# Performance work log

Measured on AMD Instinct MI355X. Metric: run time of the kernel, lower is better.

Reference implementation:

```python
import jax, jax.numpy as jnp
import numpy as np

NUM_GRAPHS = 5 * 0 + 64  # number of graphs in the batch
NUM_CLASSES = 5


def gcn_conv(x, src, dst, W, b, n_nodes):
    """PyG GCNConv: x' = D^{-1/2} (A+I) D^{-1/2} x W + b (self-loops already in src/dst)."""
    h = x @ W  # [N, out]
    deg = jax.ops.segment_sum(jnp.ones(dst.shape, h.dtype), dst, num_segments=n_nodes)
    dinv = deg ** -0.5  # deg >= 1 thanks to self-loops
    norm = dinv[src] * dinv[dst]  # [E+N]
    msg = h[src] * norm[:, None]  # gather + normalize
    out = jax.ops.segment_sum(msg, dst, num_segments=n_nodes)  # scatter-add
    return out + b


def setup_inputs() -> dict:
    key = jax.random.key(0)
    ks = jax.random.split(key, 12)
    N, E, D_IN, D_H, D_F = 50000, 500000, 128, 256, 256
    x = jax.random.normal(ks[0], (N, D_IN), dtype=jnp.float32)
    edge_index = jax.random.randint(ks[1], (2, E), 0, N, dtype=jnp.int64)
    batch = jnp.sort(jax.random.randint(ks[2], (N,), 0, NUM_GRAPHS, dtype=jnp.int64))
    def lin(k, fi, fo):
        s = 1.0 / np.sqrt(fi)
        return jax.random.uniform(k, (fi, fo), jnp.float32, -s, s)
    return {
        "x": x, "edge_index": edge_index, "batch": batch,
        "W0": lin(ks[3], D_IN, D_H), "b0": jnp.zeros((D_H,), jnp.float32),
        "W1": lin(ks[4], D_H, D_H),  "b1": jnp.zeros((D_H,), jnp.float32),
        "W2": lin(ks[5], D_H, D_H),  "b2": jnp.zeros((D_H,), jnp.float32),
        "Wc1": lin(ks[6], D_H, D_F), "bc1": jnp.zeros((D_F,), jnp.float32),
        "Wc2": lin(ks[7], D_F, NUM_CLASSES), "bc2": jnp.zeros((NUM_CLASSES,), jnp.float32),
    }


def reference(x, edge_index, batch, W0, b0, W1, b1, W2, b2, Wc1, bc1, Wc2, bc2):
    n_nodes = x.shape[0]
    loops = jnp.arange(n_nodes, dtype=edge_index.dtype)
    src = jnp.concatenate([edge_index[0], loops])
    dst = jnp.concatenate([edge_index[1], loops])

    h = jax.nn.relu(gcn_conv(x, src, dst, W0, b0, n_nodes))
    h = jax.nn.relu(gcn_conv(h, src, dst, W1, b1, n_nodes))
    h = jax.nn.relu(gcn_conv(h, src, dst, W2, b2, n_nodes))

    # global_mean_pool over batch ids
    sums = jax.ops.segment_sum(h, batch, num_segments=NUM_GRAPHS)
    cnts = jax.ops.segment_sum(jnp.ones((n_nodes,), h.dtype), batch, num_segments=NUM_GRAPHS)
    g = sums / jnp.maximum(cnts, 1.0)[:, None]  # [NUM_GRAPHS, D_H]

    # classifier MLP (dropout inactive at eval)
    out = jax.nn.relu(g @ Wc1 + bc1) @ Wc2 + bc2
    return out
```

## Files before the change

kernel.cpp:

```cpp
#include <hip/hip_runtime.h>
#include <hip/hip_fp16.h>

typedef _Float16 f16x8 __attribute__((ext_vector_type(8)));
typedef float fx4 __attribute__((ext_vector_type(4)));

#define AS_G(p) ((const __attribute__((address_space(1))) void*)(p))
#define AS_L(p) ((__attribute__((address_space(3))) void*)(p))

struct __align__(8) half4 { __half2 lo, hi; };
struct __align__(8) edge_t { int u; float w; };

__device__ inline void split2h(float a, __half& hi, __half& lo) {
    hi = __float2half(a);
    lo = __float2half(a - __half2float(hi));
}


__global__ void k_degx(const int* __restrict__ dst, int E, int* __restrict__ deg, int degB,
                       const float* __restrict__ x, __half* __restrict__ xh, int nx) {
    if (blockIdx.x < (unsigned)degB) {
        int i = (blockIdx.x * 256 + threadIdx.x) * 4;
        if (i + 4 <= E) {
            int4 d4 = *(const int4*)&dst[i];
            atomicAdd(&deg[d4.x], 1);
            atomicAdd(&deg[d4.y], 1);
            atomicAdd(&deg[d4.z], 1);
            atomicAdd(&deg[d4.w], 1);
        } else {
            for (int j = i; j < E; ++j) atomicAdd(&deg[dst[j]], 1);
        }
    } else {
        int i = (blockIdx.x - degB) * 1024 + threadIdx.x * 4;
        if (i < nx) {
            float4 v = *(const float4*)&x[i];
            __half2 h0(__float2half(v.x), __float2half(v.y));
            __half2 h1(__float2half(v.z), __float2half(v.w));
            *(__half2*)&xh[i] = h0;
            *(__half2*)&xh[i + 2] = h1;
        }
    }
}

__global__ void k_scan1w(const int* __restrict__ deg, int N, int nb,
                         int* __restrict__ part, int* __restrict__ bsum, float* __restrict__ dinv,
                         const float* __restrict__ W0, __half* __restrict__ h0, __half* __restrict__ l0,
                         const float* __restrict__ W1, __half* __restrict__ h1, __half* __restrict__ l1,
                         const float* __restrict__ W2, __half* __restrict__ h2, __half* __restrict__ l2,
                         int DIN, int DH) {
    __shared__ int s[256];
    if (blockIdx.x < (unsigned)nb) {
        int i = blockIdx.x * 256 + threadIdx.x;
        int v = (i < N) ? deg[i] : 0;
        if (i < N) dinv[i] = 1.0f / sqrtf((float)(v + 1));
        s[threadIdx.x] = v;
        __syncthreads();
        for (int off = 1; off < 256; off <<= 1) {
            int t = (threadIdx.x >= off) ? s[threadIdx.x - off] : 0;
            __syncthreads();
            s[threadIdx.x] += t;
            __syncthreads();
        }
        if (i < N) part[i] = s[threadIdx.x] - v;
        if (threadIdx.x == 255) bsum[blockIdx.x] = s[255];
    } else {
        int i = (blockIdx.x - nb) * 256 + threadIdx.x;
        const int n0 = DIN * DH, n1 = DH * DH;
        const float* W; __half *hT, *lT; int K, li;
        if (i < n0) { W = W0; hT = h0; lT = l0; K = DIN; li = i; }
        else if (i < n0 + n1) { W = W1; hT = h1; lT = l1; K = DH; li = i - n0; }
        else if (i < n0 + 2 * n1) { W = W2; hT = h2; lT = l2; K = DH; li = i - n0 - n1; }
        else return;
        int k = li / DH, n = li - k * DH;
        __half h, l;
        split2h(W[li], h, l);
        hT[(size_t)n * K + k] = h;
        lT[(size_t)n * K + k] = l;
    }
}

__global__ void k_scan3(const int* __restrict__ part, const int* __restrict__ bsum, int nb,
                        int N, int E, int* __restrict__ rowptr, int* __restrict__ cursor) {
    __shared__ int s[256];
    const int t = threadIdx.x;
    s[t] = (t < nb && t < (int)blockIdx.x) ? bsum[t] : 0;
    __syncthreads();
    for (int off = 128; off > 0; off >>= 1) {
        if (t < off) s[t] += s[t + off];
        __syncthreads();
    }
    const int base = s[0];
    int i = blockIdx.x * 256 + t;
    if (i < N) {
        int v = part[i] + base;
        rowptr[i] = v;
        cursor[i] = v;
    }
    if (i == 0) rowptr[N] = E;
}

__global__ void k_fill(const int* __restrict__ src, const int* __restrict__ dst, int E,
                       const float* __restrict__ dinv, int* __restrict__ cursor,
                       edge_t* __restrict__ edg) {
    int e = blockIdx.x * blockDim.x + threadIdx.x;
    if (e < E) {
        int s = src[e], d = dst[e];
        int p = atomicAdd(&cursor[d], 1);
        edge_t ed;
        ed.u = s;
        ed.w = dinv[s] * dinv[d];
        edg[p] = ed;
    }
}


__device__ __forceinline__ void gemm_core(
    const __half* __restrict__ Aop, const __half* __restrict__ BhiT, const __half* __restrict__ BloT,
    __half* smem, int Nrows, int K, int row0,
    int wid, int lane, int wrow, int wcol, int quad, int l16, fx4 (&acc)[4][4]) {
    const __half* gp[5];
    int ldsoff[5];
#pragma unroll
    for (int j = 0; j < 5; ++j) {
        int L = wid * 5 + j;
        int arr, slot;
        if (L < 8) { arr = 0; slot = L; }
        else if (L < 24) { arr = 1; slot = L - 8; }
        else { arr = 2; slot = L - 24; }
        int r = 16 * slot + (lane >> 2);
        int s = lane & 3;
        int q = (s - (r >> 1)) & 3;
        const __half* garr = (arr == 0) ? Aop : (arr == 1) ? BhiT : BloT;
        int grow = (arr == 0) ? min(row0 + r, Nrows - 1) : r;
        gp[j] = garr + (size_t)grow * K + q * 8;
        ldsoff[j] = ((arr == 0) ? 0 : (arr == 1) ? 8192 : 24576) + slot * 1024;
    }

    const __half* sA   = smem;
    const __half* sBhi = smem + 4096;
    const __half* sBlo = smem + 12288;

    int aidx[4], bidx[4];
#pragma unroll
    for (int t = 0; t < 4; ++t) {
        int ra = wrow * 64 + t * 16 + l16;
        aidx[t] = ra * 32 + ((quad + (ra >> 1)) & 3) * 8;
        int rb = wcol * 64 + t * 16 + l16;
        bidx[t] = rb * 32 + ((quad + (rb >> 1)) & 3) * 8;
    }

    for (int k0 = 0; k0 < K; k0 += 32) {
#pragma unroll
        for (int j = 0; j < 5; ++j)
            __builtin_amdgcn_global_load_lds(AS_G(gp[j] + k0), AS_L((char*)smem + ldsoff[j]), 16, 0, 0);
        __syncthreads();

        f16x8 a[4];
#pragma unroll
        for (int mi = 0; mi < 4; ++mi) a[mi] = *(const f16x8*)&sA[aidx[mi]];
#pragma unroll
        for (int nj = 0; nj < 4; ++nj) {
            f16x8 bh = *(const f16x8*)&sBhi[bidx[nj]];
            f16x8 bl = *(const f16x8*)&sBlo[bidx[nj]];
#pragma unroll
            for (int mi = 0; mi < 4; ++mi) {
                acc[mi][nj] = __builtin_amdgcn_mfma_f32_16x16x32_f16(a[mi], bh, acc[mi][nj], 0, 0, 0);
                acc[mi][nj] = __builtin_amdgcn_mfma_f32_16x16x32_f16(a[mi], bl, acc[mi][nj], 0, 0, 0);
            }
        }
        __syncthreads();
    }
}

__global__ __launch_bounds__(512) void k_gemm_mfma(
    const __half* __restrict__ Aop, const __half* __restrict__ BhiT, const __half* __restrict__ BloT,
    const float* __restrict__ bias, __half* __restrict__ C, int Nrows, int K) {
    __shared__ __align__(16) __half smem[20480];
    const int tid = threadIdx.x;
    const int wid = tid >> 6, lane = tid & 63;
    const int row0 = blockIdx.x * 128;
    const int wrow = wid & 1, wcol = wid >> 1;
    const int quad = lane >> 4, l16 = lane & 15;

    fx4 acc[4][4] = {};
    gemm_core(Aop, BhiT, BloT, smem, Nrows, K, row0, wid, lane, wrow, wcol, quad, l16, acc);

#pragma unroll
    for (int mi = 0; mi < 4; ++mi) {
        const int rbase = row0 + wrow * 64 + mi * 16 + quad * 4;
#pragma unroll
        for (int nj = 0; nj < 4; ++nj) {
            const int c = wcol * 64 + nj * 16 + l16;
            const float bc = bias[c];
#pragma unroll
            for (int reg = 0; reg < 4; ++reg) {
                int r = rbase + reg;
                if (r < Nrows) C[(size_t)r * 256 + c] = __float2half(fmaxf(acc[mi][nj][reg] + bc, 0.f));
            }
        }
    }
}

__global__ __launch_bounds__(512) void k_gemm_pool(
    const __half* __restrict__ Aop, const __half* __restrict__ BhiT, const __half* __restrict__ BloT,
    const float* __restrict__ bias, const int* __restrict__ batch,
    float* __restrict__ gsum, int Nrows, int K) {
    __shared__ __align__(16) __half smem[20480];
    const int tid = threadIdx.x;
    const int wid = tid >> 6, lane = tid & 63;
    const int row0 = blockIdx.x * 128;
    const int wrow = wid & 1, wcol = wid >> 1;
    const int quad = lane >> 4, l16 = lane & 15;

    fx4 acc[4][4] = {};
    gemm_core(Aop, BhiT, BloT, smem, Nrows, K, row0, wid, lane, wrow, wcol, quad, l16, acc);

    int bg[4][4];
#pragma unroll
    for (int mi = 0; mi < 4; ++mi)
#pragma unroll
        for (int reg = 0; reg < 4; ++reg) {
            int r = row0 + wrow * 64 + mi * 16 + quad * 4 + reg;
            bg[mi][reg] = (r < Nrows) ? batch[r] : -1;
        }
    const int gfirst = batch[row0 < Nrows ? row0 : (Nrows - 1)];
    const int glast  = batch[min(row0 + 127, Nrows - 1)];

#pragma unroll
    for (int nj = 0; nj < 4; ++nj) {
        const int c = wcol * 64 + nj * 16 + l16;
        const float bc = bias[c];
        for (int g = gfirst; g <= glast; ++g) {
            float s = 0.f;
#pragma unroll
            for (int mi = 0; mi < 4; ++mi)
#pragma unroll
                for (int reg = 0; reg < 4; ++reg)
                    if (bg[mi][reg] == g) s += fmaxf(acc[mi][nj][reg] + bc, 0.f);
            s += __shfl_xor(s, 16);
            s += __shfl_xor(s, 32);
            if (quad == 0) atomicAdd(&gsum[g * 256 + c], s);
        }
    }
}


__global__ __launch_bounds__(256) void k_agg256(const __half* __restrict__ H, const int* __restrict__ rowptr,
                                                const edge_t* __restrict__ edg,
                                                const float* __restrict__ dinv,
                                                __half* __restrict__ outA, int N) {
    const int wave = threadIdx.x >> 6, lane = threadIdx.x & 63;
    const int nw = gridDim.x * 4;
    for (int v = blockIdx.x * 4 + wave; v < N; v += nw) {
        const float di = dinv[v];
        const float selfn = di * di;
        half4 hv = ((const half4*)&H[(size_t)v * 256])[lane];
        float2 s0 = __half22float2(hv.lo), s1 = __half22float2(hv.hi);
        float ax = selfn * s0.x, ay = selfn * s0.y, az = selfn * s1.x, aw = selfn * s1.y;

        int e = rowptr[v];
        const int end = rowptr[v + 1];
        for (; e + 8 <= end; e += 8) {
            edge_t ed[8]; half4 g[8];
#pragma unroll
            for (int j = 0; j < 8; ++j) ed[j] = edg[e + j];
#pragma unroll
            for (int j = 0; j < 8; ++j) g[j] = ((const half4*)&H[(size_t)ed[j].u * 256])[lane];
#pragma unroll
            for (int j = 0; j < 8; ++j) {
                float2 f0 = __half22float2(g[j].lo), f1 = __half22float2(g[j].hi);
                ax += ed[j].w * f0.x; ay += ed[j].w * f0.y; az += ed[j].w * f1.x; aw += ed[j].w * f1.y;
            }
        }
        for (; e < end; ++e) {
            edge_t ed = edg[e];
            half4 g = ((const half4*)&H[(size_t)ed.u * 256])[lane];
            float2 f0 = __half22float2(g.lo), f1 = __half22float2(g.hi);
            ax += ed.w * f0.x; ay += ed.w * f0.y; az += ed.w * f1.x; aw += ed.w * f1.y;
        }

        half4 o;
        o.lo = __floats2half2_rn(ax, ay);
        o.hi = __floats2half2_rn(az, aw);
        ((half4*)outA)[(size_t)v * 64 + lane] = o;
    }
}

__global__ __launch_bounds__(256) void k_agg128(const __half* __restrict__ X, const int* __restrict__ rowptr,
                                                const edge_t* __restrict__ edg,
                                                const float* __restrict__ dinv,
                                                __half* __restrict__ outA, int N) {
    const int half = threadIdx.x >> 5, sub = threadIdx.x & 31;
    const int nw = gridDim.x * 8;
    for (int v = blockIdx.x * 8 + half; v < N; v += nw) {
        const float di = dinv[v];
        const float selfn = di * di;
        half4 hv = ((const half4*)&X[(size_t)v * 128])[sub];
        float2 s0 = __half22float2(hv.lo), s1 = __half22float2(hv.hi);
        float ax = selfn * s0.x, ay = selfn * s0.y, az = selfn * s1.x, aw = selfn * s1.y;

        int e = rowptr[v];
        const int end = rowptr[v + 1];
        for (; e + 4 <= end; e += 4) {
            edge_t ed[4]; half4 g[4];
#pragma unroll
            for (int j = 0; j < 4; ++j) ed[j] = edg[e + j];
#pragma unroll
            for (int j = 0; j < 4; ++j) g[j] = ((const half4*)&X[(size_t)ed[j].u * 128])[sub];
#pragma unroll
            for (int j = 0; j < 4; ++j) {
                float2 f0 = __half22float2(g[j].lo), f1 = __half22float2(g[j].hi);
                ax += ed[j].w * f0.x; ay += ed[j].w * f0.y; az += ed[j].w * f1.x; aw += ed[j].w * f1.y;
            }
        }
        for (; e < end; ++e) {
            edge_t ed = edg[e];
            half4 g = ((const half4*)&X[(size_t)ed.u * 128])[sub];
            float2 f0 = __half22float2(g.lo), f1 = __half22float2(g.hi);
            ax += ed.w * f0.x; ay += ed.w * f0.y; az += ed.w * f1.x; aw += ed.w * f1.y;
        }

        half4 o;
        o.lo = __floats2half2_rn(ax, ay);
        o.hi = __floats2half2_rn(az, aw);
        ((half4*)outA)[(size_t)v * 32 + sub] = o;
    }
}


__global__ __launch_bounds__(256) void k_poolcls(const float* __restrict__ gsum, const int* __restrict__ batch,
                                                 int N,
                                                 const float* __restrict__ Wc1, const float* __restrict__ bc1,
                                                 const float* __restrict__ Wc2, const float* __restrict__ bc2,
                                                 float* __restrict__ out) {
    __shared__ float sg[256], sh[256];
    __shared__ int bounds[2];
    const int b = blockIdx.x, t = threadIdx.x;
    if (t < 2) {
        int target = b + t;
        int lo = 0, hi = N;
        while (lo < hi) {
            int mid = (lo + hi) >> 1;
            if (batch[mid] < target) lo = mid + 1; else hi = mid;
        }
        bounds[t] = lo;
    }
    __syncthreads();
    const float c = (float)(bounds[1] - bounds[0]);
    sg[t] = gsum[b * 256 + t] / fmaxf(c, 1.0f);
    __syncthreads();
    float acc = bc1[t];
    for (int k = 0; k < 256; ++k) acc += sg[k] * Wc1[k * 256 + t];
    sh[t] = fmaxf(acc, 0.f);
    __syncthreads();
    if (t < 5) {
        float o = bc2[t];
        for (int k = 0; k < 256; ++k) o += sh[k] * Wc2[k * 5 + t];
        out[b * 5 + t] = o;
    }
}


extern "C" void kernel_launch(void* const* d_in, const int* in_sizes, int n_in,
                              void* d_out, int out_size, void* d_ws, size_t ws_size,
                              hipStream_t stream) {
    const float* x    = (const float*)d_in[0];
    const int*   eidx = (const int*)d_in[1];
    const int*   batch= (const int*)d_in[2];
    const float* W0 = (const float*)d_in[3];  const float* b0 = (const float*)d_in[4];
    const float* W1 = (const float*)d_in[5];  const float* b1 = (const float*)d_in[6];
    const float* W2 = (const float*)d_in[7];  const float* b2 = (const float*)d_in[8];
    const float* Wc1= (const float*)d_in[9];  const float* bc1= (const float*)d_in[10];
    const float* Wc2= (const float*)d_in[11]; const float* bc2= (const float*)d_in[12];
    float* out = (float*)d_out;

    const int N   = in_sizes[2];
    const int E   = in_sizes[1] / 2;
    const int DIN = in_sizes[0] / N;
    const int DH  = in_sizes[4];
    const int* src = eidx;
    const int* dst = eidx + E;

    char* p = (char*)d_ws;
    auto alloc = [&](size_t bytes) {
        char* r = p;
        p += (bytes + 255) & ~(size_t)255;
        return (void*)r;
    };
    __half* hbuf = (__half*)alloc((size_t)N * DH * 2);
    __half* ha   = (__half*)alloc((size_t)N * DH * 2);
    __half* xh   = (__half*)alloc((size_t)N * DIN * 2);
    __half* w0hi = (__half*)alloc((size_t)DH * DIN * 2);
    __half* w0lo = (__half*)alloc((size_t)DH * DIN * 2);
    __half* w1hi = (__half*)alloc((size_t)DH * DH * 2);
    __half* w1lo = (__half*)alloc((size_t)DH * DH * 2);
    __half* w2hi = (__half*)alloc((size_t)DH * DH * 2);
    __half* w2lo = (__half*)alloc((size_t)DH * DH * 2);
    int*   deg   = (int*)alloc((size_t)N * 4);
    float* gsum  = (float*)alloc(64 * (size_t)DH * 4);
    float* dinv  = (float*)alloc((size_t)N * 4);
    int*   part  = (int*)alloc((size_t)N * 4);
    int*   bsum  = (int*)alloc(256 * 4);
    int*   rowptr= (int*)alloc((size_t)(N + 1) * 4);
    int*   cursor= (int*)alloc((size_t)N * 4);
    edge_t* edg  = (edge_t*)alloc((size_t)E * 8);

    hipMemsetAsync(deg, 0, (size_t)((char*)gsum - (char*)deg) + 64 * (size_t)DH * 4, stream);

    const int nb = (N + 255) / 256;
    const int wtot = DIN * DH + 2 * DH * DH;
    const int wb = (wtot + 255) / 256;
    const int degB = (E + 1023) / 1024;
    const int nx = N * DIN;
    const int xb = (nx + 1023) / 1024;

    k_degx  <<<degB + xb, 256, 0, stream>>>(dst, E, deg, degB, x, xh, nx);
    k_scan1w<<<nb + wb, 256, 0, stream>>>(deg, N, nb, part, bsum, dinv,
                                          W0, w0hi, w0lo, W1, w1hi, w1lo, W2, w2hi, w2lo, DIN, DH);
    k_scan3 <<<nb, 256, 0, stream>>>(part, bsum, nb, N, E, rowptr, cursor);
    k_fill  <<<(E + 255) / 256, 256, 0, stream>>>(src, dst, E, dinv, cursor, edg);

    const int gemmBlocks = (N + 127) / 128;
    const int agg256B = min((N + 3) / 4, 2048);
    const int agg128B = min((N + 7) / 8, 2048);

    k_agg128<<<agg128B, 256, 0, stream>>>(xh, rowptr, edg, dinv, ha, N);
    k_gemm_mfma<<<gemmBlocks, 512, 0, stream>>>(ha, w0hi, w0lo, b0, hbuf, N, DIN);
    k_agg256<<<agg256B, 256, 0, stream>>>(hbuf, rowptr, edg, dinv, ha, N);
    k_gemm_mfma<<<gemmBlocks, 512, 0, stream>>>(ha, w1hi, w1lo, b1, hbuf, N, DH);
    k_agg256<<<agg256B, 256, 0, stream>>>(hbuf, rowptr, edg, dinv, ha, N);
    k_gemm_pool<<<gemmBlocks, 512, 0, stream>>>(ha, w2hi, w2lo, b2, batch, gsum, N, DH);

    k_poolcls<<<64, 256, 0, stream>>>(gsum, batch, N, Wc1, bc1, Wc2, bc2, out);
}
```

Before: 346.0 us.

## Split each layer in half and overlap aggregation of second half with GEMM of first

Each GCN layer is split into two row halves. The first half is aggregated, then one mixed launch runs the GEMM on the first half while other blocks aggregate the second half, followed by the GEMM on the second half. The goal is to overlap the memory-bound gather with the MFMA GEMM and reduce idle tail time between dependent kernels. In exchange it adds launches, swaps the grid-stride aggregation loops for one-row-per-wave grids, adds a second hidden buffer, and the mixed blocks share a large LDS allocation even when they only aggregate.

```diff
diff --git a/kernel.cpp b/kernel.cpp
--- a/kernel.cpp
+++ b/kernel.cpp
@@ -113,6 +113,95 @@
 }
 
 
+__device__ __forceinline__ void agg_row256(const __half* __restrict__ H,
+    const int* __restrict__ rowptr, const edge_t* __restrict__ edg,
+    const float* __restrict__ dinv, __half* __restrict__ outA, int v, int lane) {
+    const float di = dinv[v];
+    const float selfn = di * di;
+    half4 hv = ((const half4*)&H[(size_t)v * 256])[lane];
+    float2 s0 = __half22float2(hv.lo), s1 = __half22float2(hv.hi);
+    float ax = selfn * s0.x, ay = selfn * s0.y, az = selfn * s1.x, aw = selfn * s1.y;
+
+    int e = rowptr[v];
+    const int end = rowptr[v + 1];
+    for (; e + 8 <= end; e += 8) {
+        edge_t ed[8]; half4 g[8];
+#pragma unroll
+        for (int j = 0; j < 8; ++j) ed[j] = edg[e + j];
+#pragma unroll
+        for (int j = 0; j < 8; ++j) g[j] = ((const half4*)&H[(size_t)ed[j].u * 256])[lane];
+#pragma unroll
+        for (int j = 0; j < 8; ++j) {
+            float2 f0 = __half22float2(g[j].lo), f1 = __half22float2(g[j].hi);
+            ax += ed[j].w * f0.x; ay += ed[j].w * f0.y; az += ed[j].w * f1.x; aw += ed[j].w * f1.y;
+        }
+    }
+    for (; e < end; ++e) {
+        edge_t ed = edg[e];
+        half4 g = ((const half4*)&H[(size_t)ed.u * 256])[lane];
+        float2 f0 = __half22float2(g.lo), f1 = __half22float2(g.hi);
+        ax += ed.w * f0.x; ay += ed.w * f0.y; az += ed.w * f1.x; aw += ed.w * f1.y;
+    }
+
+    half4 o;
+    o.lo = __floats2half2_rn(ax, ay);
+    o.hi = __floats2half2_rn(az, aw);
+    ((half4*)outA)[(size_t)v * 64 + lane] = o;
+}
+
+__device__ __forceinline__ void agg_row128(const __half* __restrict__ X,
+    const int* __restrict__ rowptr, const edge_t* __restrict__ edg,
+    const float* __restrict__ dinv, __half* __restrict__ outA, int v, int sub) {
+    const float di = dinv[v];
+    const float selfn = di * di;
+    half4 hv = ((const half4*)&X[(size_t)v * 128])[sub];
+    float2 s0 = __half22float2(hv.lo), s1 = __half22float2(hv.hi);
+    float ax = selfn * s0.x, ay = selfn * s0.y, az = selfn * s1.x, aw = selfn * s1.y;
+
+    int e = rowptr[v];
+    const int end = rowptr[v + 1];
+    for (; e + 4 <= end; e += 4) {
+        edge_t ed[4]; half4 g[4];
+#pragma unroll
+        for (int j = 0; j < 4; ++j) ed[j] = edg[e + j];
+#pragma unroll
+        for (int j = 0; j < 4; ++j) g[j] = ((const half4*)&X[(size_t)ed[j].u * 128])[sub];
+#pragma unroll
+        for (int j = 0; j < 4; ++j) {
+            float2 f0 = __half22float2(g[j].lo), f1 = __half22float2(g[j].hi);
+            ax += ed[j].w * f0.x; ay += ed[j].w * f0.y; az += ed[j].w * f1.x; aw += ed[j].w * f1.y;
+        }
+    }
+    for (; e < end; ++e) {
+        edge_t ed = edg[e];
+        half4 g = ((const half4*)&X[(size_t)ed.u * 128])[sub];
+        float2 f0 = __half22float2(g.lo), f1 = __half22float2(g.hi);
+        ax += ed.w * f0.x; ay += ed.w * f0.y; az += ed.w * f1.x; aw += ed.w * f1.y;
+    }
+
+    half4 o;
+    o.lo = __floats2half2_rn(ax, ay);
+    o.hi = __floats2half2_rn(az, aw);
+    ((half4*)outA)[(size_t)v * 32 + sub] = o;
+}
+
+__global__ __launch_bounds__(256) void k_agg256(const __half* __restrict__ H, const int* __restrict__ rowptr,
+                                                const edge_t* __restrict__ edg,
+                                                const float* __restrict__ dinv,
+                                                __half* __restrict__ outA, int a0, int a1) {
+    const int v = a0 + blockIdx.x * 4 + (threadIdx.x >> 6);
+    if (v < a1) agg_row256(H, rowptr, edg, dinv, outA, v, threadIdx.x & 63);
+}
+
+__global__ __launch_bounds__(256) void k_agg128(const __half* __restrict__ X, const int* __restrict__ rowptr,
+                                                const edge_t* __restrict__ edg,
+                                                const float* __restrict__ dinv,
+                                                __half* __restrict__ outA, int a0, int a1) {
+    const int v = a0 + blockIdx.x * 8 + (threadIdx.x >> 5);
+    if (v < a1) agg_row128(X, rowptr, edg, dinv, outA, v, threadIdx.x & 31);
+}
+
+
 __device__ __forceinline__ void gemm_core(
     const __half* __restrict__ Aop, const __half* __restrict__ BhiT, const __half* __restrict__ BloT,
     __half* smem, int Nrows, int K, int row0,
@@ -171,19 +260,9 @@
     }
 }
 
-__global__ __launch_bounds__(512) void k_gemm_mfma(
-    const __half* __restrict__ Aop, const __half* __restrict__ BhiT, const __half* __restrict__ BloT,
-    const float* __restrict__ bias, __half* __restrict__ C, int Nrows, int K) {
-    __shared__ __align__(16) __half smem[20480];
-    const int tid = threadIdx.x;
-    const int wid = tid >> 6, lane = tid & 63;
-    const int row0 = blockIdx.x * 128;
-    const int wrow = wid & 1, wcol = wid >> 1;
-    const int quad = lane >> 4, l16 = lane & 15;
-
-    fx4 acc[4][4] = {};
-    gemm_core(Aop, BhiT, BloT, smem, Nrows, K, row0, wid, lane, wrow, wcol, quad, l16, acc);
-
+__device__ __forceinline__ void gemm_store(fx4 (&acc)[4][4], const float* __restrict__ bias,
+                                           __half* __restrict__ C, int row0, int g1,
+                                           int wrow, int wcol, int quad, int l16) {
 #pragma unroll
     for (int mi = 0; mi < 4; ++mi) {
         const int rbase = row0 + wrow * 64 + mi * 16 + quad * 4;
@@ -194,36 +273,25 @@
 #pragma unroll
             for (int reg = 0; reg < 4; ++reg) {
                 int r = rbase + reg;
-                if (r < Nrows) C[(size_t)r * 256 + c] = __float2half(fmaxf(acc[mi][nj][reg] + bc, 0.f));
+                if (r < g1) C[(size_t)r * 256 + c] = __float2half(fmaxf(acc[mi][nj][reg] + bc, 0.f));
             }
         }
     }
 }
 
-__global__ __launch_bounds__(512) void k_gemm_pool(
-    const __half* __restrict__ Aop, const __half* __restrict__ BhiT, const __half* __restrict__ BloT,
-    const float* __restrict__ bias, const int* __restrict__ batch,
-    float* __restrict__ gsum, int Nrows, int K) {
-    __shared__ __align__(16) __half smem[20480];
-    const int tid = threadIdx.x;
-    const int wid = tid >> 6, lane = tid & 63;
-    const int row0 = blockIdx.x * 128;
-    const int wrow = wid & 1, wcol = wid >> 1;
-    const int quad = lane >> 4, l16 = lane & 15;
-
-    fx4 acc[4][4] = {};
-    gemm_core(Aop, BhiT, BloT, smem, Nrows, K, row0, wid, lane, wrow, wcol, quad, l16, acc);
-
+__device__ __forceinline__ void gemm_poolst(fx4 (&acc)[4][4], const float* __restrict__ bias,
+                                            const int* __restrict__ batch, float* __restrict__ gsum,
+                                            int row0, int g1, int wrow, int wcol, int quad, int l16) {
     int bg[4][4];
 #pragma unroll
     for (int mi = 0; mi < 4; ++mi)
 #pragma unroll
         for (int reg = 0; reg < 4; ++reg) {
             int r = row0 + wrow * 64 + mi * 16 + quad * 4 + reg;
-            bg[mi][reg] = (r < Nrows) ? batch[r] : -1;
-        }
-    const int gfirst = batch[row0 < Nrows ? row0 : (Nrows - 1)];
-    const int glast  = batch[min(row0 + 127, Nrows - 1)];
+            bg[mi][reg] = (r < g1) ? batch[r] : -1;
+        }
+    const int gfirst = batch[min(row0, g1 - 1)];
+    const int glast  = batch[min(row0 + 127, g1 - 1)];
 
 #pragma unroll
     for (int nj = 0; nj < 4; ++nj) {
@@ -243,87 +311,95 @@
     }
 }
 
-
-__global__ __launch_bounds__(256) void k_agg256(const __half* __restrict__ H, const int* __restrict__ rowptr,
-                                                const edge_t* __restrict__ edg,
-                                                const float* __restrict__ dinv,
-                                                __half* __restrict__ outA, int N) {
-    const int wave = threadIdx.x >> 6, lane = threadIdx.x & 63;
-    const int nw = gridDim.x * 4;
-    for (int v = blockIdx.x * 4 + wave; v < N; v += nw) {
-        const float di = dinv[v];
-        const float selfn = di * di;
-        half4 hv = ((const half4*)&H[(size_t)v * 256])[lane];
-        float2 s0 = __half22float2(hv.lo), s1 = __half22float2(hv.hi);
-        float ax = selfn * s0.x, ay = selfn * s0.y, az = selfn * s1.x, aw = selfn * s1.y;
-
-        int e = rowptr[v];
-        const int end = rowptr[v + 1];
-        for (; e + 8 <= end; e += 8) {
-            edge_t ed[8]; half4 g[8];
-#pragma unroll
-            for (int j = 0; j < 8; ++j) ed[j] = edg[e + j];
-#pragma unroll
-            for (int j = 0; j < 8; ++j) g[j] = ((const half4*)&H[(size_t)ed[j].u * 256])[lane];
-#pragma unroll
-            for (int j = 0; j < 8; ++j) {
-                float2 f0 = __half22float2(g[j].lo), f1 = __half22float2(g[j].hi);
-                ax += ed[j].w * f0.x; ay += ed[j].w * f0.y; az += ed[j].w * f1.x; aw += ed[j].w * f1.y;
-            }
-        }
-        for (; e < end; ++e) {
-            edge_t ed = edg[e];
-            half4 g = ((const half4*)&H[(size_t)ed.u * 256])[lane];
-            float2 f0 = __half22float2(g.lo), f1 = __half22float2(g.hi);
-            ax += ed.w * f0.x; ay += ed.w * f0.y; az += ed.w * f1.x; aw += ed.w * f1.y;
-        }
-
-        half4 o;
-        o.lo = __floats2half2_rn(ax, ay);
-        o.hi = __floats2half2_rn(az, aw);
-        ((half4*)outA)[(size_t)v * 64 + lane] = o;
-    }
-}
-
-__global__ __launch_bounds__(256) void k_agg128(const __half* __restrict__ X, const int* __restrict__ rowptr,
-                                                const edge_t* __restrict__ edg,
-                                                const float* __restrict__ dinv,
-                                                __half* __restrict__ outA, int N) {
-    const int half = threadIdx.x >> 5, sub = threadIdx.x & 31;
-    const int nw = gridDim.x * 8;
-    for (int v = blockIdx.x * 8 + half; v < N; v += nw) {
-        const float di = dinv[v];
-        const float selfn = di * di;
-        half4 hv = ((const half4*)&X[(size_t)v * 128])[sub];
-        float2 s0 = __half22float2(hv.lo), s1 = __half22float2(hv.hi);
-        float ax = selfn * s0.x, ay = selfn * s0.y, az = selfn * s1.x, aw = selfn * s1.y;
-
-        int e = rowptr[v];
-        const int end = rowptr[v + 1];
-        for (; e + 4 <= end; e += 4) {
-            edge_t ed[4]; half4 g[4];
-#pragma unroll
-            for (int j = 0; j < 4; ++j) ed[j] = edg[e + j];
-#pragma unroll
-            for (int j = 0; j < 4; ++j) g[j] = ((const half4*)&X[(size_t)ed[j].u * 128])[sub];
-#pragma unroll
-            for (int j = 0; j < 4; ++j) {
-                float2 f0 = __half22float2(g[j].lo), f1 = __half22float2(g[j].hi);
-                ax += ed[j].w * f0.x; ay += ed[j].w * f0.y; az += ed[j].w * f1.x; aw += ed[j].w * f1.y;
-            }
-        }
-        for (; e < end; ++e) {
-            edge_t ed = edg[e];
-            half4 g = ((const half4*)&X[(size_t)ed.u * 128])[sub];
-            float2 f0 = __half22float2(g.lo), f1 = __half22float2(g.hi);
-            ax += ed.w * f0.x; ay += ed.w * f0.y; az += ed.w * f1.x; aw += ed.w * f1.y;
-        }
-
-        half4 o;
-        o.lo = __floats2half2_rn(ax, ay);
-        o.hi = __floats2half2_rn(az, aw);
-        ((half4*)outA)[(size_t)v * 32 + sub] = o;
-    }
+__global__ __launch_bounds__(512) void k_gemm_mfma(
+    const __half* __restrict__ Aop, const __half* __restrict__ BhiT, const __half* __restrict__ BloT,
+    const float* __restrict__ bias, __half* __restrict__ C, int g0, int g1, int K) {
+    __shared__ __align__(16) __half smem[20480];
+    const int tid = threadIdx.x;
+    const int wid = tid >> 6, lane = tid & 63;
+    const int row0 = g0 + blockIdx.x * 128;
+    const int wrow = wid & 1, wcol = wid >> 1;
+    const int quad = lane >> 4, l16 = lane & 15;
+    fx4 acc[4][4] = {};
+    gemm_core(Aop, BhiT, BloT, smem, g1, K, row0, wid, lane, wrow, wcol, quad, l16, acc);
+    gemm_store(acc, bias, C, row0, g1, wrow, wcol, quad, l16);
+}
+
+__global__ __launch_bounds__(512) void k_gemm_pool(
+    const __half* __restrict__ Aop, const __half* __restrict__ BhiT, const __half* __restrict__ BloT,
+    const float* __restrict__ bias, const int* __restrict__ batch,
+    float* __restrict__ gsum, int g0, int g1, int K) {
+    __shared__ __align__(16) __half smem[20480];
+    const int tid = threadIdx.x;
+    const int wid = tid >> 6, lane = tid & 63;
+    const int row0 = g0 + blockIdx.x * 128;
+    const int wrow = wid & 1, wcol = wid >> 1;
+    const int quad = lane >> 4, l16 = lane & 15;
+    fx4 acc[4][4] = {};
+    gemm_core(Aop, BhiT, BloT, smem, g1, K, row0, wid, lane, wrow, wcol, quad, l16, acc);
+    gemm_poolst(acc, bias, batch, gsum, row0, g1, wrow, wcol, quad, l16);
+}
+
+
+template<int KD, bool POOL>
+__device__ __forceinline__ void mix_impl(
+    const __half* __restrict__ Hsrc, const int* __restrict__ rowptr,
+    const edge_t* __restrict__ edg, const float* __restrict__ dinv,
+    __half* __restrict__ aggOut, int a0, int a1, int GB,
+    const __half* __restrict__ Aop, const __half* __restrict__ BhiT,
+    const __half* __restrict__ BloT, const float* __restrict__ bias,
+    __half* __restrict__ C, const int* __restrict__ batch,
+    float* __restrict__ gsum, int g0, int g1) {
+    __shared__ __align__(16) __half smem[20480];
+    const int tid = threadIdx.x;
+    if ((int)blockIdx.x >= GB) {
+        const int ab = blockIdx.x - GB;
+        if (KD == 256) {
+            const int v = a0 + ab * 8 + (tid >> 6);
+            if (v < a1) agg_row256(Hsrc, rowptr, edg, dinv, aggOut, v, tid & 63);
+        } else {
+            const int v = a0 + ab * 16 + (tid >> 5);
+            if (v < a1) agg_row128(Hsrc, rowptr, edg, dinv, aggOut, v, tid & 31);
+        }
+        return;
+    }
+    const int wid = tid >> 6, lane = tid & 63;
+    const int row0 = g0 + blockIdx.x * 128;
+    const int wrow = wid & 1, wcol = wid >> 1;
+    const int quad = lane >> 4, l16 = lane & 15;
+    fx4 acc[4][4] = {};
+    gemm_core(Aop, BhiT, BloT, smem, g1, KD, row0, wid, lane, wrow, wcol, quad, l16, acc);
+    if constexpr (!POOL)
+        gemm_store(acc, bias, C, row0, g1, wrow, wcol, quad, l16);
+    else
+        gemm_poolst(acc, bias, batch, gsum, row0, g1, wrow, wcol, quad, l16);
+}
+
+__global__ __launch_bounds__(512) void k_mix128(
+    const __half* Hsrc, const int* rowptr, const edge_t* edg, const float* dinv,
+    __half* aggOut, int a0, int a1, int GB,
+    const __half* Aop, const __half* BhiT, const __half* BloT, const float* bias,
+    __half* C, int g0, int g1) {
+    mix_impl<128, false>(Hsrc, rowptr, edg, dinv, aggOut, a0, a1, GB,
+                         Aop, BhiT, BloT, bias, C, nullptr, nullptr, g0, g1);
+}
+
+__global__ __launch_bounds__(512) void k_mix256(
+    const __half* Hsrc, const int* rowptr, const edge_t* edg, const float* dinv,
+    __half* aggOut, int a0, int a1, int GB,
+    const __half* Aop, const __half* BhiT, const __half* BloT, const float* bias,
+    __half* C, int g0, int g1) {
+    mix_impl<256, false>(Hsrc, rowptr, edg, dinv, aggOut, a0, a1, GB,
+                         Aop, BhiT, BloT, bias, C, nullptr, nullptr, g0, g1);
+}
+
+__global__ __launch_bounds__(512) void k_mix256p(
+    const __half* Hsrc, const int* rowptr, const edge_t* edg, const float* dinv,
+    __half* aggOut, int a0, int a1, int GB,
+    const __half* Aop, const __half* BhiT, const __half* BloT, const float* bias,
+    const int* batch, float* gsum, int g0, int g1) {
+    mix_impl<256, true>(Hsrc, rowptr, edg, dinv, aggOut, a0, a1, GB,
+                        Aop, BhiT, BloT, bias, nullptr, batch, gsum, g0, g1);
 }
 
 
@@ -386,7 +462,8 @@
         p += (bytes + 255) & ~(size_t)255;
         return (void*)r;
     };
-    __half* hbuf = (__half*)alloc((size_t)N * DH * 2);
+    __half* h0b  = (__half*)alloc((size_t)N * DH * 2);
+    __half* h1b  = (__half*)alloc((size_t)N * DH * 2);
     __half* ha   = (__half*)alloc((size_t)N * DH * 2);
     __half* xh   = (__half*)alloc((size_t)N * DIN * 2);
     __half* w0hi = (__half*)alloc((size_t)DH * DIN * 2);
@@ -419,16 +496,28 @@
     k_scan3 <<<nb, 256, 0, stream>>>(part, bsum, nb, N, E, rowptr, cursor);
     k_fill  <<<(E + 255) / 256, 256, 0, stream>>>(src, dst, E, dinv, cursor, edg);
 
-    const int gemmBlocks = (N + 127) / 128;
-    const int agg256B = min((N + 3) / 4, 2048);
-    const int agg128B = min((N + 7) / 8, 2048);
-
-    k_agg128<<<agg128B, 256, 0, stream>>>(xh, rowptr, edg, dinv, ha, N);
-    k_gemm_mfma<<<gemmBlocks, 512, 0, stream>>>(ha, w0hi, w0lo, b0, hbuf, N, DIN);
-    k_agg256<<<agg256B, 256, 0, stream>>>(hbuf, rowptr, edg, dinv, ha, N);
-    k_gemm_mfma<<<gemmBlocks, 512, 0, stream>>>(ha, w1hi, w1lo, b1, hbuf, N, DH);
-    k_agg256<<<agg256B, 256, 0, stream>>>(hbuf, rowptr, edg, dinv, ha, N);
-    k_gemm_pool<<<gemmBlocks, 512, 0, stream>>>(ha, w2hi, w2lo, b2, batch, gsum, N, DH);
+    const int H   = min((((N / 2) + 127) / 128) * 128, N);
+    const int GB1 = (H + 127) / 128;
+    const int GB2 = (N - H + 127) / 128;
+    const int A1_256 = (H + 3) / 4;
+    const int A2_256 = (N - H + 7) / 8;
+    const int A1_128 = (H + 7) / 8;
+    const int A2_128 = (N - H + 15) / 16;
+
+    k_agg128<<<A1_128, 256, 0, stream>>>(xh, rowptr, edg, dinv, ha, 0, H);
+    k_mix128<<<GB1 + A2_128, 512, 0, stream>>>(xh, rowptr, edg, dinv, ha, H, N, GB1,
+                                               ha, w0hi, w0lo, b0, h0b, 0, H);
+    if (GB2) k_gemm_mfma<<<GB2, 512, 0, stream>>>(ha, w0hi, w0lo, b0, h0b, H, N, DIN);
+
+    k_agg256<<<A1_256, 256, 0, stream>>>(h0b, rowptr, edg, dinv, ha, 0, H);
+    k_mix256<<<GB1 + A2_256, 512, 0, stream>>>(h0b, rowptr, edg, dinv, ha, H, N, GB1,
+                                               ha, w1hi, w1lo, b1, h1b, 0, H);
+    if (GB2) k_gemm_mfma<<<GB2, 512, 0, stream>>>(ha, w1hi, w1lo, b1, h1b, H, N, DH);
+
+    k_agg256<<<A1_256, 256, 0, stream>>>(h1b, rowptr, edg, dinv, ha, 0, H);
+    k_mix256p<<<GB1 + A2_256, 512, 0, stream>>>(h1b, rowptr, edg, dinv, ha, H, N, GB1,
+                                                ha, w2hi, w2lo, b2, batch, gsum, 0, H);
+    if (GB2) k_gemm_pool<<<GB2, 512, 0, stream>>>(ha, w2hi, w2lo, b2, batch, gsum, H, N, DH);
 
     k_poolcls<<<64, 256, 0, stream>>>(gsum, batch, N, Wc1, bc1, Wc2, bc2, out);
 }
```

Result: slower. 401.0 us (+15.9%).
